# Performance work log

Measured on AMD Instinct MI355X. Metric: run time of the kernel, lower is better.

The kernel has to match this reference:

```python
import jax, jax.numpy as jnp
import numpy as np

N_NODES = 50000
N_EDGES = 800000
D_FEAT = 64      # input_size
D_OUT = 64       # output_size
N_REL = 8
N_BASES = 4


def setup_inputs() -> dict:
    key = jax.random.key(0)
    k1, k2, k3, k4, k5, k6 = jax.random.split(key, 6)
    x = jax.random.normal(k1, (N_NODES, D_FEAT, N_REL), dtype=jnp.float32)
    edge_src = jax.random.randint(k2, (N_EDGES,), 0, N_NODES, dtype=jnp.int32)
    edge_dst = jax.random.randint(k3, (N_EDGES,), 0, N_NODES, dtype=jnp.int32)
    edge_weight = jax.random.uniform(k4, (N_EDGES,), dtype=jnp.float32)
    # basis-decomposed relation weights (xavier-like scale)
    w_bases = jax.random.normal(k5, (N_BASES, D_FEAT, D_OUT), dtype=jnp.float32) * (2.0 / (D_FEAT + D_OUT)) ** 0.5
    w_rel = jax.random.normal(k6, (N_REL, N_BASES), dtype=jnp.float32) * (2.0 / (N_REL + N_BASES)) ** 0.5
    return {"x": x, "edge_src": edge_src, "edge_dst": edge_dst,
            "edge_weight": edge_weight, "w_bases": w_bases, "w_rel": w_rel}


def reference(x, edge_src, edge_dst, edge_weight, w_bases, w_rel):
    # w[r] = sum_b w_rel[r,b] * w_bases[b]  -> [R, d_in, d_out]
    w = jnp.einsum('rb,bio->rio', w_rel, w_bases)
    n_rel = x.shape[-1]
    n_nodes = x.shape[0]
    # sparse adjacency message passing per relation: support_r = A @ x[:, :, r]
    # A @ y == segment_sum over edges (dst <- weight * y[src])
    supports = []
    for r in range(n_rel):  # small fixed relation count
        msgs = edge_weight[:, None] * x[edge_src, :, r]          # [E, d_in]
        agg = jax.ops.segment_sum(msgs, edge_dst, num_segments=n_nodes)  # [N, d_in]
        supports.append(agg)
    tmp = jnp.concatenate(supports, axis=1)                      # [N, R*d_in]
    weights = w.reshape(n_rel * x.shape[1], w.shape[2])          # [R*d_in, d_out]
    out = tmp @ weights                                          # [N, d_out]
    return out
```

## Files before the change

kernel.cpp:

```cpp
#include <hip/hip_runtime.h>
#include <hip/hip_bf16.h>

#define DFEAT   64
#define NREL    8
#define KDIM    512
#define DOUT    64
#define NBASES  4

#define CHSZ    128
#define NCB_MAX 400
#define OVFC    400
#define EPB     2048
#define CAPB    8
#define SORTMX  2944

typedef short short8 __attribute__((ext_vector_type(8)));
typedef float f32x4  __attribute__((ext_vector_type(4)));
typedef unsigned short ushort8 __attribute__((ext_vector_type(8)));

__device__ __forceinline__ unsigned short f2bf(float f) {
    unsigned u = __float_as_uint(f);
    u += 0x7fff + ((u >> 16) & 1);
    return (unsigned short)(u >> 16);
}
__device__ __forceinline__ float bf2f(unsigned short b) {
    return __uint_as_float(((unsigned)b) << 16);
}

__global__ __launch_bounds__(256) void weight_kernel(
    const float* __restrict__ w_rel,
    const float* __restrict__ w_bases,
    unsigned short* __restrict__ wT,
    int* __restrict__ cursor)
{
    int idx = blockIdx.x * 256 + threadIdx.x;
    int k = idx & 511;
    int o = idx >> 9;
    int i = k >> 3;
    int r = k & 7;
    float s = 0.f;
#pragma unroll
    for (int b = 0; b < NBASES; ++b)
        s += w_rel[r * NBASES + b] * w_bases[(b * DFEAT + i) * DOUT + o];
    wT[o * KDIM + k] = f2bf(s);

    if (idx < OVFC + 8) cursor[idx] = 0;
}

union SharedK2 {
    unsigned short ylds[4][16][64];
    struct {
        uint2 bin[NCB_MAX][CAPB];
        int bcnt[NCB_MAX];
    } b;
};

__global__ __launch_bounds__(256) void fused_kernel(
    const float* __restrict__ x,
    const unsigned short* __restrict__ wT,
    unsigned short* __restrict__ y,
    int n_nodes,
    const int* __restrict__ esrc, const int* __restrict__ edst,
    const float* __restrict__ ew,
    int* __restrict__ cursor,
    uint2* __restrict__ slab, uint2* __restrict__ ovf,
    int n_edges, int nc, int slab_cap, int ovf_cap, int t_blocks)
{
    const int tid = threadIdx.x;
    __shared__ SharedK2 sh;

    if (blockIdx.x >= t_blocks) {
        auto& B = sh.b;
        const int lim = nc < NCB_MAX ? nc : NCB_MAX;
        for (int i = tid; i < lim; i += 256) B.bcnt[i] = 0;
        __syncthreads();

        int e0 = (blockIdx.x - t_blocks) * EPB + tid;
#pragma unroll
        for (int j = 0; j < EPB / 256; ++j) {
            int e = e0 + j * 256;
            if (e < n_edges) {
                int d = edst[e];
                unsigned entry = (unsigned)(esrc[e] & 0xFFFF)
                               | ((unsigned)f2bf(ew[e]) << 16);
                int c = d >> 7;
                uint2 rec = make_uint2(entry, (unsigned)d);
                int pos = (c < NCB_MAX) ? atomicAdd(&B.bcnt[c], 1) : CAPB;
                if (pos < CAPB) {
                    B.bin[c][pos] = rec;
                } else {
                    int p = atomicAdd(&cursor[c], 1);
                    if (p < slab_cap) slab[(size_t)c * slab_cap + p] = rec;
                    else { int q = atomicAdd(&cursor[OVFC], 1);
                           if (q < ovf_cap) ovf[q] = rec; }
                }
            }
        }
        __syncthreads();

        for (int c = tid; c < lim; c += 256) {
            int n = B.bcnt[c]; if (n > CAPB) n = CAPB;
            int bb = atomicAdd(&cursor[c], n);
            uint2* sc = slab + (size_t)c * slab_cap;
            for (int i = 0; i < n; ++i) {
                uint2 rec = B.bin[c][i];
                int p = bb + i;
                if (p < slab_cap) sc[p] = rec;
                else { int q = atomicAdd(&cursor[OVFC], 1);
                       if (q < ovf_cap) ovf[q] = rec; }
            }
        }
        return;
    }

    const int wid  = tid >> 6;
    const int lane = tid & 63;
    const int quad = lane >> 4;
    const int fi   = lane & 15;

    const int node0 = (blockIdx.x * 4 + wid) * 16;
    int myrow = node0 + fi;
    if (myrow >= n_nodes) myrow = n_nodes - 1;
    const float* xg = x + (size_t)myrow * KDIM + quad * 8;
    const unsigned short* wg = wT + fi * KDIM + quad * 8;

    f32x4 acc0 = {0.f, 0.f, 0.f, 0.f};
    f32x4 acc1 = {0.f, 0.f, 0.f, 0.f};
    f32x4 acc2 = {0.f, 0.f, 0.f, 0.f};
    f32x4 acc3 = {0.f, 0.f, 0.f, 0.f};

#pragma unroll 4
    for (int kb = 0; kb < KDIM; kb += 32) {
        float4 xa = *(const float4*)(xg + kb);
        float4 xb = *(const float4*)(xg + kb + 4);
        short8 a;
        a[0] = f2bf(xa.x); a[1] = f2bf(xa.y); a[2] = f2bf(xa.z); a[3] = f2bf(xa.w);
        a[4] = f2bf(xb.x); a[5] = f2bf(xb.y); a[6] = f2bf(xb.z); a[7] = f2bf(xb.w);

        short8 b0 = *(const short8*)(wg + kb);
        short8 b1 = *(const short8*)(wg + 16 * KDIM + kb);
        short8 b2 = *(const short8*)(wg + 32 * KDIM + kb);
        short8 b3 = *(const short8*)(wg + 48 * KDIM + kb);

        acc0 = __builtin_amdgcn_mfma_f32_16x16x32_bf16(a, b0, acc0, 0, 0, 0);
        acc1 = __builtin_amdgcn_mfma_f32_16x16x32_bf16(a, b1, acc1, 0, 0, 0);
        acc2 = __builtin_amdgcn_mfma_f32_16x16x32_bf16(a, b2, acc2, 0, 0, 0);
        acc3 = __builtin_amdgcn_mfma_f32_16x16x32_bf16(a, b3, acc3, 0, 0, 0);
    }

#pragma unroll
    for (int r = 0; r < 4; ++r) {
        int n = quad * 4 + r;
        sh.ylds[wid][n][fi]      = f2bf(acc0[r]);
        sh.ylds[wid][n][16 + fi] = f2bf(acc1[r]);
        sh.ylds[wid][n][32 + fi] = f2bf(acc2[r]);
        sh.ylds[wid][n][48 + fi] = f2bf(acc3[r]);
    }
    __syncthreads();

    int nl = lane >> 2;
    int cg = (lane & 3) * 16;
    int node = node0 + nl;
    if (node < n_nodes) {
        ushort8 v0 = *(const ushort8*)&sh.ylds[wid][nl][cg];
        ushort8 v1 = *(const ushort8*)&sh.ylds[wid][nl][cg + 8];
        unsigned short* yr = y + (size_t)node * DOUT + cg;
        *(ushort8*)yr       = v0;
        *(ushort8*)(yr + 8) = v1;
    }
}

__global__ __launch_bounds__(1024, 4) void aggregate_kernel(
    const uint2* __restrict__ slab, const uint2* __restrict__ ovf,
    const int* __restrict__ cursor,
    const unsigned short* __restrict__ y,
    float* __restrict__ out, int n_nodes,
    int slab_cap, int ovf_cap)
{
    __shared__ unsigned sorted[SORTMX];
    __shared__ int hist[CHSZ];
    __shared__ int start[CHSZ + 1];
    __shared__ int cur[CHSZ];

    const int tid = threadIdx.x;
    const int c = blockIdx.x;
    const int nbase = c * CHSZ;
    int nspan = CHSZ;
    if (nspan > n_nodes - nbase) nspan = n_nodes - nbase;
    if (nspan <= 0) return;

    if (tid < CHSZ) hist[tid] = 0;
    __syncthreads();

    int total = cursor[c]; if (total > slab_cap) total = slab_cap;
    const uint2* sl = slab + (size_t)c * slab_cap;

    for (int i = tid; i < total; i += 1024)
        atomicAdd(&hist[(int)sl[i].y - nbase], 1);
    __syncthreads();

    if (tid < 64) {
        int a = hist[2 * tid], b = hist[2 * tid + 1];
        int v = a + b;
#pragma unroll
        for (int off = 1; off < 64; off <<= 1) {
            int t = __shfl_up(v, off);
            if (tid >= off) v += t;
        }
        int excl = v - (a + b);
        start[2 * tid]     = excl;
        start[2 * tid + 1] = excl + a;
        cur[2 * tid]       = excl;
        cur[2 * tid + 1]   = excl + a;
        if (tid == 63) start[CHSZ] = v;
    }
    __syncthreads();

    for (int i = tid; i < total; i += 1024) {
        uint2 rec = sl[i];
        int pos = atomicAdd(&cur[(int)rec.y - nbase], 1);
        sorted[pos] = rec.x;
    }
    __syncthreads();

    const int lane = tid & 63;
    const int wv   = tid >> 6;
    const int s    = lane >> 3;
    const int f    = lane & 7;
    int novf = cursor[OVFC]; if (novf > ovf_cap) novf = ovf_cap;

    for (int rel = wv; rel < nspan; rel += 16) {
        int s0 = start[rel], s1 = start[rel + 1];
        float a[8];
#pragma unroll
        for (int j = 0; j < 8; ++j) a[j] = 0.f;

        for (int k = s0 + s; k < s1; k += 8) {
            unsigned e = sorted[k];
            float w = __uint_as_float(e & 0xFFFF0000u);
            ushort8 yv = *(const ushort8*)(y + (size_t)(e & 0xFFFFu) * DOUT + f * 8);
#pragma unroll
            for (int j = 0; j < 8; ++j) a[j] += w * bf2f(yv[j]);
        }

        if (novf > 0) {
            for (int i = s; i < novf; i += 8) {
                uint2 rec = ovf[i];
                if ((int)rec.y == nbase + rel) {
                    float w = __uint_as_float(rec.x & 0xFFFF0000u);
                    const unsigned short* yr =
                        y + (size_t)(rec.x & 0xFFFFu) * DOUT + f * 8;
#pragma unroll
                    for (int j = 0; j < 8; ++j) a[j] += w * bf2f(yr[j]);
                }
            }
        }

#pragma unroll
        for (int m = 8; m <= 32; m <<= 1)
#pragma unroll
            for (int j = 0; j < 8; ++j) a[j] += __shfl_xor(a[j], m);

        if (s == 0) {
            float* orow = out + (size_t)(nbase + rel) * DOUT + f * 8;
            *(float4*)orow       = make_float4(a[0], a[1], a[2], a[3]);
            *(float4*)(orow + 4) = make_float4(a[4], a[5], a[6], a[7]);
        }
    }
}

extern "C" void kernel_launch(void* const* d_in, const int* in_sizes, int n_in,
                              void* d_out, int out_size, void* d_ws, size_t ws_size,
                              hipStream_t stream) {
    const float* x       = (const float*)d_in[0];
    const int*   esrc    = (const int*)d_in[1];
    const int*   edst    = (const int*)d_in[2];
    const float* ew      = (const float*)d_in[3];
    const float* w_bases = (const float*)d_in[4];
    const float* w_rel   = (const float*)d_in[5];
    float* out = (float*)d_out;

    const int n_nodes = in_sizes[0] / KDIM;
    const int n_edges = in_sizes[1];
    const int nc = (n_nodes + CHSZ - 1) / CHSZ;

    size_t wsw = ws_size / 4;
    size_t base = (size_t)n_nodes * 32 + 16384 + 416;
    size_t avail = (wsw > base) ? wsw - base : 0;
    size_t slab_budget = avail * 7 / 8;
    int slab_cap = (int)(slab_budget / (2 * (size_t)nc));
    if (slab_cap > SORTMX) slab_cap = SORTMX;
    size_t ovf_words = avail - (size_t)2 * nc * slab_cap;
    size_t oc = ovf_words / 2;
    int ovf_cap = (int)(oc > (size_t)n_edges ? (size_t)n_edges : oc);

    unsigned short* y   = (unsigned short*)d_ws;
    unsigned short* wT  = y + (size_t)n_nodes * DOUT;
    int*   cursor       = (int*)(wT + KDIM * DOUT);
    uint2* slab         = (uint2*)(cursor + 416);
    uint2* ovf          = slab + (size_t)nc * slab_cap;

    weight_kernel<<<(KDIM * DOUT) / 256, 256, 0, stream>>>(
        w_rel, w_bases, wT, cursor);

    const int t_blocks = (n_nodes + 63) / 64;
    const int p_blocks = (n_edges + EPB - 1) / EPB;
    fused_kernel<<<t_blocks + p_blocks, 256, 0, stream>>>(
        x, wT, y, n_nodes,
        esrc, edst, ew, cursor, slab, ovf,
        n_edges, nc, slab_cap, ovf_cap, t_blocks);

    aggregate_kernel<<<nc, 1024, 0, stream>>>(
        slab, ovf, cursor, y, out, n_nodes, slab_cap, ovf_cap);
}
```

Measured before the change: 224.2 us.

## Pad atomic cursors, schedule partition blocks first, prefetch x in transform GEMM

Cursor counters are spread to one per 128-byte stride so global atomics from different chunks no longer share cache lines. The edge-partition blocks now get the low block indices, so they are dispatched before the dense transform blocks and can overlap with them. The per-block LDS bin capacity rises from 8 to 12 to send fewer records down the global-atomic spill path. The transform loop is restructured to software-prefetch the next 128-wide slice of x while the current slice goes through the MFMAs. This costs more registers and a larger shared-memory union, which may lower occupancy.

After: 224.7 us. No clear change (+0.2%).

```diff
diff --git a/kernel.cpp b/kernel.cpp
--- a/kernel.cpp
+++ b/kernel.cpp
@@ -10,8 +10,9 @@
 #define CHSZ    128
 #define NCB_MAX 400
 #define OVFC    400
+#define CSTR    32
 #define EPB     2048
-#define CAPB    8
+#define CAPB    12
 #define SORTMX  2944
 
 typedef short short8 __attribute__((ext_vector_type(8)));
@@ -44,7 +45,7 @@
         s += w_rel[r * NBASES + b] * w_bases[(b * DFEAT + i) * DOUT + o];
     wT[o * KDIM + k] = f2bf(s);
 
-    if (idx < OVFC + 8) cursor[idx] = 0;
+    if (idx < (OVFC + 8) * CSTR) cursor[idx] = 0;
 }
 
 union SharedK2 {
@@ -64,18 +65,18 @@
     const float* __restrict__ ew,
     int* __restrict__ cursor,
     uint2* __restrict__ slab, uint2* __restrict__ ovf,
-    int n_edges, int nc, int slab_cap, int ovf_cap, int t_blocks)
+    int n_edges, int nc, int slab_cap, int ovf_cap, int p_blocks)
 {
     const int tid = threadIdx.x;
     __shared__ SharedK2 sh;
 
-    if (blockIdx.x >= t_blocks) {
+    if (blockIdx.x < p_blocks) {
         auto& B = sh.b;
         const int lim = nc < NCB_MAX ? nc : NCB_MAX;
         for (int i = tid; i < lim; i += 256) B.bcnt[i] = 0;
         __syncthreads();
 
-        int e0 = (blockIdx.x - t_blocks) * EPB + tid;
+        int e0 = blockIdx.x * EPB + tid;
 #pragma unroll
         for (int j = 0; j < EPB / 256; ++j) {
             int e = e0 + j * 256;
@@ -89,9 +90,9 @@
                 if (pos < CAPB) {
                     B.bin[c][pos] = rec;
                 } else {
-                    int p = atomicAdd(&cursor[c], 1);
+                    int p = atomicAdd(&cursor[c * CSTR], 1);
                     if (p < slab_cap) slab[(size_t)c * slab_cap + p] = rec;
-                    else { int q = atomicAdd(&cursor[OVFC], 1);
+                    else { int q = atomicAdd(&cursor[OVFC * CSTR], 1);
                            if (q < ovf_cap) ovf[q] = rec; }
                 }
             }
@@ -100,25 +101,26 @@
 
         for (int c = tid; c < lim; c += 256) {
             int n = B.bcnt[c]; if (n > CAPB) n = CAPB;
-            int bb = atomicAdd(&cursor[c], n);
+            int bb = atomicAdd(&cursor[c * CSTR], n);
             uint2* sc = slab + (size_t)c * slab_cap;
             for (int i = 0; i < n; ++i) {
                 uint2 rec = B.bin[c][i];
                 int p = bb + i;
                 if (p < slab_cap) sc[p] = rec;
-                else { int q = atomicAdd(&cursor[OVFC], 1);
+                else { int q = atomicAdd(&cursor[OVFC * CSTR], 1);
                        if (q < ovf_cap) ovf[q] = rec; }
             }
         }
         return;
     }
 
+    const int bidx = blockIdx.x - p_blocks;
     const int wid  = tid >> 6;
     const int lane = tid & 63;
     const int quad = lane >> 4;
     const int fi   = lane & 15;
 
-    const int node0 = (blockIdx.x * 4 + wid) * 16;
+    const int node0 = (bidx * 4 + wid) * 16;
     int myrow = node0 + fi;
     if (myrow >= n_nodes) myrow = n_nodes - 1;
     const float* xg = x + (size_t)myrow * KDIM + quad * 8;
@@ -129,23 +131,44 @@
     f32x4 acc2 = {0.f, 0.f, 0.f, 0.f};
     f32x4 acc3 = {0.f, 0.f, 0.f, 0.f};
 
-#pragma unroll 4
-    for (int kb = 0; kb < KDIM; kb += 32) {
-        float4 xa = *(const float4*)(xg + kb);
-        float4 xb = *(const float4*)(xg + kb + 4);
-        short8 a;
-        a[0] = f2bf(xa.x); a[1] = f2bf(xa.y); a[2] = f2bf(xa.z); a[3] = f2bf(xa.w);
-        a[4] = f2bf(xb.x); a[5] = f2bf(xb.y); a[6] = f2bf(xb.z); a[7] = f2bf(xb.w);
-
-        short8 b0 = *(const short8*)(wg + kb);
-        short8 b1 = *(const short8*)(wg + 16 * KDIM + kb);
-        short8 b2 = *(const short8*)(wg + 32 * KDIM + kb);
-        short8 b3 = *(const short8*)(wg + 48 * KDIM + kb);
-
-        acc0 = __builtin_amdgcn_mfma_f32_16x16x32_bf16(a, b0, acc0, 0, 0, 0);
-        acc1 = __builtin_amdgcn_mfma_f32_16x16x32_bf16(a, b1, acc1, 0, 0, 0);
-        acc2 = __builtin_amdgcn_mfma_f32_16x16x32_bf16(a, b2, acc2, 0, 0, 0);
-        acc3 = __builtin_amdgcn_mfma_f32_16x16x32_bf16(a, b3, acc3, 0, 0, 0);
+    float4 xa0, xa1, xa2, xa3, xb0, xb1, xb2, xb3;
+    xa0 = *(const float4*)(xg +   0); xb0 = *(const float4*)(xg +   4);
+    xa1 = *(const float4*)(xg +  32); xb1 = *(const float4*)(xg +  36);
+    xa2 = *(const float4*)(xg +  64); xb2 = *(const float4*)(xg +  68);
+    xa3 = *(const float4*)(xg +  96); xb3 = *(const float4*)(xg + 100);
+
+#pragma unroll 1
+    for (int km = 0; km < KDIM; km += 128) {
+        float4 na0, na1, na2, na3, nb0, nb1, nb2, nb3;
+        if (km + 128 < KDIM) {
+            const float* xn = xg + km + 128;
+            na0 = *(const float4*)(xn +   0); nb0 = *(const float4*)(xn +   4);
+            na1 = *(const float4*)(xn +  32); nb1 = *(const float4*)(xn +  36);
+            na2 = *(const float4*)(xn +  64); nb2 = *(const float4*)(xn +  68);
+            na3 = *(const float4*)(xn +  96); nb3 = *(const float4*)(xn + 100);
+        }
+#define XSTEP(XA, XB, U)                                                      \
+        {                                                                     \
+            short8 a;                                                         \
+            a[0]=f2bf(XA.x); a[1]=f2bf(XA.y); a[2]=f2bf(XA.z); a[3]=f2bf(XA.w);\
+            a[4]=f2bf(XB.x); a[5]=f2bf(XB.y); a[6]=f2bf(XB.z); a[7]=f2bf(XB.w);\
+            int kb = km + (U) * 32;                                           \
+            short8 b0 = *(const short8*)(wg + kb);                            \
+            short8 b1 = *(const short8*)(wg + 16 * KDIM + kb);                \
+            short8 b2 = *(const short8*)(wg + 32 * KDIM + kb);                \
+            short8 b3 = *(const short8*)(wg + 48 * KDIM + kb);                \
+            acc0 = __builtin_amdgcn_mfma_f32_16x16x32_bf16(a, b0, acc0, 0,0,0);\
+            acc1 = __builtin_amdgcn_mfma_f32_16x16x32_bf16(a, b1, acc1, 0,0,0);\
+            acc2 = __builtin_amdgcn_mfma_f32_16x16x32_bf16(a, b2, acc2, 0,0,0);\
+            acc3 = __builtin_amdgcn_mfma_f32_16x16x32_bf16(a, b3, acc3, 0,0,0);\
+        }
+        XSTEP(xa0, xb0, 0)
+        XSTEP(xa1, xb1, 1)
+        XSTEP(xa2, xb2, 2)
+        XSTEP(xa3, xb3, 3)
+#undef XSTEP
+        xa0 = na0; xb0 = nb0; xa1 = na1; xb1 = nb1;
+        xa2 = na2; xb2 = nb2; xa3 = na3; xb3 = nb3;
     }
 
 #pragma unroll
@@ -192,7 +215,7 @@
     if (tid < CHSZ) hist[tid] = 0;
     __syncthreads();
 
-    int total = cursor[c]; if (total > slab_cap) total = slab_cap;
+    int total = cursor[c * CSTR]; if (total > slab_cap) total = slab_cap;
     const uint2* sl = slab + (size_t)c * slab_cap;
 
     for (int i = tid; i < total; i += 1024)
@@ -227,7 +250,7 @@
     const int wv   = tid >> 6;
     const int s    = lane >> 3;
     const int f    = lane & 7;
-    int novf = cursor[OVFC]; if (novf > ovf_cap) novf = ovf_cap;
+    int novf = cursor[OVFC * CSTR]; if (novf > ovf_cap) novf = ovf_cap;
 
     for (int rel = wv; rel < nspan; rel += 16) {
         int s0 = start[rel], s1 = start[rel + 1];
@@ -283,9 +306,10 @@
     const int n_nodes = in_sizes[0] / KDIM;
     const int n_edges = in_sizes[1];
     const int nc = (n_nodes + CHSZ - 1) / CHSZ;
+    const int cwords = (OVFC + 8) * CSTR;
 
     size_t wsw = ws_size / 4;
-    size_t base = (size_t)n_nodes * 32 + 16384 + 416;
+    size_t base = (size_t)n_nodes * 32 + 16384 + cwords;
     size_t avail = (wsw > base) ? wsw - base : 0;
     size_t slab_budget = avail * 7 / 8;
     int slab_cap = (int)(slab_budget / (2 * (size_t)nc));
@@ -297,7 +321,7 @@
     unsigned short* y   = (unsigned short*)d_ws;
     unsigned short* wT  = y + (size_t)n_nodes * DOUT;
     int*   cursor       = (int*)(wT + KDIM * DOUT);
-    uint2* slab         = (uint2*)(cursor + 416);
+    uint2* slab         = (uint2*)(cursor + cwords);
     uint2* ovf          = slab + (size_t)nc * slab_cap;
 
     weight_kernel<<<(KDIM * DOUT) / 256, 256, 0, stream>>>(
@@ -305,10 +329,10 @@
 
     const int t_blocks = (n_nodes + 63) / 64;
     const int p_blocks = (n_edges + EPB - 1) / EPB;
-    fused_kernel<<<t_blocks + p_blocks, 256, 0, stream>>>(
+    fused_kernel<<<p_blocks + t_blocks, 256, 0, stream>>>(
         x, wT, y, n_nodes,
         esrc, edst, ew, cursor, slab, ovf,
-        n_edges, nc, slab_cap, ovf_cap, t_blocks);
+        n_edges, nc, slab_cap, ovf_cap, p_blocks);
 
     aggregate_kernel<<<nc, 1024, 0, stream>>>(
         slab, ovf, cursor, y, out, n_nodes, slab_cap, ovf_cap);
```
